# Kernel tuning notes

Hardware: AMD Instinct MI355X
Metric: run time of the kernel (lower is better)

Reference implementation:

```python
import jax, jax.numpy as jnp
import numpy as np

BN_EPS = 1e-5

def _conv(x, W, b, stride, pad):
    # x: [B,C,H,W], W: [O,I,kh,kw]
    y = jax.lax.conv_general_dilated(
        x, W, window_strides=(stride, stride),
        padding=[(pad, pad), (pad, pad)],
        dimension_numbers=('NCHW', 'OIHW', 'NCHW'))
    return y + b[None, :, None, None]

def _bn(x, gamma, beta, mean, var):
    inv = gamma * jax.lax.rsqrt(var + BN_EPS)
    return x * inv[None, :, None, None] + (beta - mean * inv)[None, :, None, None]

def _haar_cD(x):
    # pywt.dwt2(x, 'haar') diagonal detail over last two axes (even H,W):
    # cD[i,j] = (x[2i,2j] - x[2i,2j+1] - x[2i+1,2j] + x[2i+1,2j+1]) / 2
    a = x[..., 0::2, 0::2]
    b = x[..., 0::2, 1::2]
    c = x[..., 1::2, 0::2]
    d = x[..., 1::2, 1::2]
    return (a - b - c + d) * 0.5

def setup_inputs() -> dict:
    key = jax.random.key(0)
    ks = jax.random.split(key, 20)
    B = 8192
    f32 = jnp.float32
    inp = {
        'x':   jax.random.normal(ks[0], (B, 3, 32, 32), dtype=f32),
        # conv1: 3 -> 32, k5 s2 p2
        'w1':  jax.random.normal(ks[1], (32, 3, 5, 5), dtype=f32) * 0.05,
        'b1':  jnp.zeros((32,), f32),
        'g1':  jnp.ones((32,), f32),
        'be1': jnp.zeros((32,), f32),
        'm1':  jax.random.normal(ks[2], (32,), dtype=f32) * 0.1,
        'v1':  jax.random.uniform(ks[3], (32,), dtype=f32, minval=0.5, maxval=1.5),
        # conv2: 32 -> 64, k3 s2 p1
        'w2':  jax.random.normal(ks[4], (64, 32, 3, 3), dtype=f32) * 0.05,
        'b2':  jnp.zeros((64,), f32),
        'g2':  jnp.ones((64,), f32),
        'be2': jnp.zeros((64,), f32),
        'm2':  jax.random.normal(ks[5], (64,), dtype=f32) * 0.1,
        'v2':  jax.random.uniform(ks[6], (64,), dtype=f32, minval=0.5, maxval=1.5),
        # attention conv: 64 -> 1, k1
        'wa':  jax.random.normal(ks[7], (1, 64, 1, 1), dtype=f32) * 0.1,
        'ba':  jnp.zeros((1,), f32),
        # decoder linears (torch Linear layout: [out, in])
        'wd1': jax.random.normal(ks[8], (512, 64 * 8 * 8), dtype=f32) * 0.02,
        'bd1': jnp.zeros((512,), f32),
        'wd2': jax.random.normal(ks[9], (128, 512), dtype=f32) * 0.04,
        'bd2': jnp.zeros((128,), f32),
    }
    return inp

def reference(x, w1, b1, g1, be1, m1, v1, w2, b2, g2, be2, m2, v2,
              wa, ba, wd1, bd1, wd2, bd2):
    # wavelet_conv stem
    h = jax.nn.relu(_bn(_conv(x, w1, b1, 2, 2), g1, be1, m1, v1))   # [B,32,16,16]
    feat = jax.nn.relu(_bn(_conv(h, w2, b2, 2, 1), g2, be2, m2, v2))  # [B,64,8,8]
    # Haar DWT diagonal-detail gate (detached in the original)
    cD = jax.lax.stop_gradient(_haar_cD(feat))                        # [B,64,4,4]
    cD_up = jnp.repeat(jnp.repeat(cD, 2, axis=-2), 2, axis=-1)        # [B,64,8,8]
    feat = feat * cD_up
    # attention gate
    attn = jax.nn.sigmoid(_conv(feat, wa, ba, 1, 0))                  # [B,1,8,8]
    feat = feat * attn
    # decode
    f = feat.reshape(feat.shape[0], -1)                               # [B,4096]
    h1 = jax.nn.relu(f @ wd1.T + bd1)                                  # [B,512]
    return jax.nn.sigmoid(h1 @ wd2.T + bd2)                            # [B,128]
```

## Files before the change

### kernel.cpp

```cpp
#include <hip/hip_runtime.h>
#include <hip/hip_bf16.h>

typedef __bf16 bf16x8 __attribute__((ext_vector_type(8)));
typedef __bf16 bf16x4 __attribute__((ext_vector_type(4)));
typedef float f32x4 __attribute__((ext_vector_type(4)));

#define BN_EPS 1e-5f

__device__ __forceinline__ void gl_lds16(const __bf16* g, __bf16* l) {
    __builtin_amdgcn_global_load_lds(
        (const __attribute__((address_space(1))) unsigned int*)g,
        (__attribute__((address_space(3))) unsigned int*)l,
        16, 0, 0);
}

__global__ __launch_bounds__(256) void prep_all_kernel(
    const float* __restrict__ wd1, __bf16* __restrict__ wd1o,
    const float* __restrict__ wd2, const float* __restrict__ w1,
    const float* __restrict__ w2,
    __bf16* __restrict__ wd2o, __bf16* __restrict__ w1o,
    __bf16* __restrict__ w2o)
{
    __shared__ float t2[64][65];
    const int tid = threadIdx.x;
    if (blockIdx.x < 512) {
        const int n = blockIdx.x;
        const float* src = wd1 + (size_t)n * 4096;
        #pragma unroll
        for (int r = 0; r < 16; ++r) {
            int j = r * 256 + tid;
            t2[j & 63][j >> 6] = src[j];
        }
        __syncthreads();
        __bf16* dst = wd1o + (size_t)n * 4096;
        #pragma unroll
        for (int r = 0; r < 16; ++r) {
            int t = r * 256 + tid;
            dst[t] = (__bf16)t2[t >> 6][t & 63];
        }
        return;
    }
    int i = (blockIdx.x - 512) * 256 + tid;
    if (i < 65536) { wd2o[i] = (__bf16)wd2[i]; return; }
    i -= 65536;
    if (i < 4096) {
        int oc = i >> 7, rem = i & 127;
        int ot = rem >> 3, j = rem & 7;
        float v = 0.f;
        if (ot < 15 && j < 5) {
            int ic = ot / 5, ky = ot % 5;
            v = w1[((oc * 3 + ic) * 5 + ky) * 5 + j];
        }
        w1o[i] = (__bf16)v;
        return;
    }
    i -= 4096;
    if (i < 18432) {
        int oc = i / 288, rem = i % 288;
        int tap = rem / 32, ic = rem % 32;
        w2o[i] = (__bf16)w2[(oc * 32 + ic) * 9 + tap];
    }
}

__global__ __launch_bounds__(256, 5) void conv_fused_kernel(
    const float* __restrict__ x,
    const __bf16* __restrict__ w1r, const float* __restrict__ b1,
    const float* __restrict__ g1, const float* __restrict__ be1,
    const float* __restrict__ m1, const float* __restrict__ v1,
    const __bf16* __restrict__ w2r, const float* __restrict__ b2,
    const float* __restrict__ g2, const float* __restrict__ be2,
    const float* __restrict__ m2, const float* __restrict__ v2,
    const float* __restrict__ wa, const float* __restrict__ ba,
    __bf16* __restrict__ f)
{
    __shared__ __align__(16) __bf16 xsb[3 * 36 * 40];
    __shared__ __align__(16) char  ubuf[23552];
    __bf16* hsf  = (__bf16*)ubuf;
    float*  feat = (float*)ubuf;
    float*  cds  = (float*)(ubuf + 17408);
    float*  atn  = (float*)(ubuf + 22528);

    const int b    = blockIdx.x;
    const int tid  = threadIdx.x;
    const int lane = tid & 63;
    const int wave = tid >> 6;
    const int lo   = lane >> 4;
    const int ln   = lane & 15;

    {
        bf16x8 z = {};
        for (int i = tid; i < 540; i += 256) *(bf16x8*)&xsb[i * 8] = z;
        if (tid < 132) {
            int pi = tid >> 2, ch = tid & 3;
            int pix = (pi < 17) ? pi : (pi - 16) * 17;
            *(bf16x8*)&hsf[pix * 40 + ch * 8] = z;
        }
    }
    __syncthreads();

    {
        const float4* xb = (const float4*)(x + (size_t)b * 3072);
        #pragma unroll
        for (int r = 0; r < 3; ++r) {
            int c = r * 256 + tid;
            int plane = c >> 8, rem = c & 255;
            int row = rem >> 3, c4 = rem & 7;
            float4 v = xb[c];
            bf16x4 h;
            h[0] = (__bf16)v.x; h[1] = (__bf16)v.y; h[2] = (__bf16)v.z; h[3] = (__bf16)v.w;
            *(bf16x4*)&xsb[plane * 1440 + (row + 2) * 40 + 4 + c4 * 4] = h;
        }
    }

    bf16x8 bw1[2][4];
    #pragma unroll
    for (int nt = 0; nt < 2; ++nt)
        #pragma unroll
        for (int s = 0; s < 4; ++s)
            bw1[nt][s] = *(const bf16x8*)(w1r + (nt * 16 + ln) * 128 + (s * 4 + lo) * 8);
    __syncthreads();

    f32x4 c1[4][2] = {};
    const unsigned int* xw = (const unsigned int*)xsb;
    #pragma unroll
    for (int s = 0; s < 4; ++s) {
        const int o  = s * 4 + lo;
        const int ic = (o * 205) >> 10;
        const int ky = o - ic * 5;
        const bool dummy = (o == 15);
        const int icc = dummy ? 2 : ic;
        #pragma unroll
        for (int mt = 0; mt < 4; ++mt) {
            const int oy  = wave * 4 + mt;
            const int row = dummy ? 35 : (2 * oy + ky);
            const int dw  = icc * 720 + row * 20 + ln + 1;
            union { unsigned int u[4]; bf16x8 v; } fa;
            fa.u[0] = xw[dw]; fa.u[1] = xw[dw + 1]; fa.u[2] = xw[dw + 2]; fa.u[3] = 0;
            #pragma unroll
            for (int nt = 0; nt < 2; ++nt)
                c1[mt][nt] = __builtin_amdgcn_mfma_f32_16x16x32_bf16(fa.v, bw1[nt][s], c1[mt][nt], 0, 0, 0);
        }
    }

    #pragma unroll
    for (int nt = 0; nt < 2; ++nt) {
        const int oc  = nt * 16 + ln;
        const float inv = g1[oc] * rsqrtf(v1[oc] + BN_EPS);
        const float bb  = be1[oc] + (b1[oc] - m1[oc]) * inv;
        #pragma unroll
        for (int mt = 0; mt < 4; ++mt) {
            const int hy = wave * 4 + mt + 1;
            #pragma unroll
            for (int r = 0; r < 4; ++r) {
                const int hx = lo * 4 + r + 1;
                hsf[(hy * 17 + hx) * 40 + oc] = (__bf16)fmaxf(c1[mt][nt][r] * inv + bb, 0.f);
            }
        }
    }

    const int wm = wave >> 1, wn = wave & 1;
    bf16x8 bw2[2][9];
    #pragma unroll
    for (int nt = 0; nt < 2; ++nt) {
        const __bf16* wp = w2r + (wn * 32 + nt * 16 + ln) * 288 + lo * 8;
        #pragma unroll
        for (int ks = 0; ks < 9; ++ks)
            bw2[nt][ks] = *(const bf16x8*)(wp + ks * 32);
    }
    __syncthreads();

    f32x4 c2[2][2] = {};
    {
        int pixbase[2];
        #pragma unroll
        for (int mt = 0; mt < 2; ++mt) {
            int p = wm * 32 + mt * 16 + ln;
            int qy = p >> 3, qx = p & 7;
            pixbase[mt] = (2 * qy * 17 + 2 * qx) * 40 + lo * 8;
        }
        #pragma unroll
        for (int ks = 0; ks < 9; ++ks) {
            const int ty = ks / 3, tx = ks % 3;
            bf16x8 af[2];
            #pragma unroll
            for (int mt = 0; mt < 2; ++mt)
                af[mt] = *(const bf16x8*)&hsf[pixbase[mt] + (ty * 17 + tx) * 40];
            #pragma unroll
            for (int mt = 0; mt < 2; ++mt)
                #pragma unroll
                for (int nt = 0; nt < 2; ++nt)
                    c2[mt][nt] = __builtin_amdgcn_mfma_f32_16x16x32_bf16(af[mt], bw2[nt][ks], c2[mt][nt], 0, 0, 0);
        }
    }
    __syncthreads();

    #pragma unroll
    for (int nt = 0; nt < 2; ++nt) {
        const int oc  = wn * 32 + nt * 16 + ln;
        const float inv = g2[oc] * rsqrtf(v2[oc] + BN_EPS);
        const float bb  = be2[oc] + (b2[oc] - m2[oc]) * inv;
        #pragma unroll
        for (int mt = 0; mt < 2; ++mt) {
            const int p0 = wm * 32 + mt * 16 + lo * 4;
            f32x4 o;
            #pragma unroll
            for (int r = 0; r < 4; ++r)
                o[r] = fmaxf(c2[mt][nt][r] * inv + bb, 0.f);
            *(f32x4*)&feat[oc * 68 + p0] = o;
        }
    }
    __syncthreads();

    {
        const int c = tid >> 2, y = tid & 3;
        const float* fr = feat + c * 68 + 16 * y;
        f32x4 t0 = *(const f32x4*)(fr);
        f32x4 t2v = *(const f32x4*)(fr + 4);
        f32x4 t1 = *(const f32x4*)(fr + 8);
        f32x4 t3 = *(const f32x4*)(fr + 12);
        f32x4 o;
        o[0] = 0.5f * (t0[0] - t0[1] - t1[0] + t1[1]);
        o[1] = 0.5f * (t0[2] - t0[3] - t1[2] + t1[3]);
        o[2] = 0.5f * (t2v[0] - t2v[1] - t3[0] + t3[1]);
        o[3] = 0.5f * (t2v[2] - t2v[3] - t3[2] + t3[3]);
        *(f32x4*)&cds[c * 20 + y * 4] = o;
    }
    __syncthreads();

    const int q  = tid & 63;
    const int g  = wave;
    const int qy2 = q >> 3, qx2 = q & 7;
    const int qq = (qy2 >> 1) * 4 + (qx2 >> 1);
    float a2[16];
    float part = 0.f;
    #pragma unroll
    for (int j = 0; j < 16; ++j) {
        int oc = g * 16 + j;
        float v = feat[oc * 68 + q] * cds[oc * 20 + qq];
        a2[j] = v;
        part += v * wa[oc];
    }
    atn[g * 64 + q] = part;
    __syncthreads();
    float s2  = atn[q] + atn[64 + q] + atn[128 + q] + atn[192 + q] + ba[0];
    float sig = 1.f / (1.f + __expf(-s2));

    bf16x8 fo0, fo1;
    #pragma unroll
    for (int j = 0; j < 8; ++j) {
        fo0[j] = (__bf16)(a2[j] * sig);
        fo1[j] = (__bf16)(a2[j + 8] * sig);
    }
    __bf16* fb = f + (size_t)b * 4096 + q * 64 + g * 16;
    *(bf16x8*)fb = fo0;
    *(bf16x8*)(fb + 8) = fo1;
}

__global__ __launch_bounds__(256, 4) void gemm1_split_kernel(
    const __bf16* __restrict__ A, const __bf16* __restrict__ B,
    float* __restrict__ P)
{
    const int K = 4096, NOUT = 512, KH = 2048;
    __shared__ __align__(16) __bf16 As[64][64];
    __shared__ __align__(16) __bf16 Bs[128][64];
    const int tid  = threadIdx.x;
    const int lane = tid & 63;
    const int wave = tid >> 6;
    const int lo = lane >> 4, ln = lane & 15;
    const int bid = blockIdx.x;
    const int swz = (bid & 7) * 128 + (bid >> 3);
    const int n0  = (swz & 3) * 128;
    const int zz  = (swz >> 2) & 1;
    const int m0  = (swz >> 3) * 64;
    const int ks0 = zz * KH;
    const int sw = ln & 7;
    f32x4 acc[4][2] = {};
    for (int k0 = ks0; k0 < ks0 + KH; k0 += 64) {
        #pragma unroll
        for (int r = 0; r < 2; ++r) {
            int i = r * 256 + tid;
            int row = i >> 3, cs = i & 7;
            gl_lds16(A + (size_t)(m0 + row) * K + k0 + (cs ^ (row & 7)) * 8, &As[0][0] + i * 8);
        }
        #pragma unroll
        for (int r = 0; r < 4; ++r) {
            int i = r * 256 + tid;
            int row = i >> 3, cs = i & 7;
            gl_lds16(B + (size_t)(n0 + row) * K + k0 + (cs ^ (row & 7)) * 8, &Bs[0][0] + i * 8);
        }
        __syncthreads();
        #pragma unroll
        for (int s = 0; s < 2; ++s) {
            const int c = s * 4 + lo;
            const int slot = (c ^ sw) * 8;
            bf16x8 af[4], bfr[2];
            #pragma unroll
            for (int mt = 0; mt < 4; ++mt)
                af[mt] = *(const bf16x8*)(&As[mt * 16 + ln][slot]);
            #pragma unroll
            for (int nt = 0; nt < 2; ++nt)
                bfr[nt] = *(const bf16x8*)(&Bs[wave * 32 + nt * 16 + ln][slot]);
            #pragma unroll
            for (int mt = 0; mt < 4; ++mt)
                #pragma unroll
                for (int nt = 0; nt < 2; ++nt)
                    acc[mt][nt] = __builtin_amdgcn_mfma_f32_16x16x32_bf16(af[mt], bfr[nt], acc[mt][nt], 0, 0, 0);
        }
        __syncthreads();
    }
    float* Pp = P + (size_t)zz * 8192 * 512;
    #pragma unroll
    for (int mt = 0; mt < 4; ++mt)
        #pragma unroll
        for (int nt = 0; nt < 2; ++nt)
            #pragma unroll
            for (int r = 0; r < 4; ++r) {
                int m = m0 + mt * 16 + lo * 4 + r;
                int n = n0 + wave * 32 + nt * 16 + ln;
                Pp[(size_t)m * NOUT + n] = acc[mt][nt][r];
            }
}

__global__ __launch_bounds__(256) void gemm1_kernel(
    const __bf16* __restrict__ A, const __bf16* __restrict__ B,
    const float* __restrict__ bias, __bf16* __restrict__ C)
{
    const int K = 4096, NOUT = 512;
    __shared__ __align__(16) __bf16 As[64][64];
    __shared__ __align__(16) __bf16 Bs[128][64];
    const int tid  = threadIdx.x;
    const int lane = tid & 63;
    const int wave = tid >> 6;
    const int lo = lane >> 4, ln = lane & 15;
    const int bid = blockIdx.x;
    const int swz = (bid & 7) * 64 + (bid >> 3);
    const int n0  = (swz & 3) * 128;
    const int m0  = (swz >> 2) * 64;
    const int sw = ln & 7;
    f32x4 acc[4][2] = {};
    for (int k0 = 0; k0 < K; k0 += 64) {
        #pragma unroll
        for (int r = 0; r < 2; ++r) {
            int i = r * 256 + tid;
            int row = i >> 3, cs = i & 7;
            gl_lds16(A + (size_t)(m0 + row) * K + k0 + (cs ^ (row & 7)) * 8, &As[0][0] + i * 8);
        }
        #pragma unroll
        for (int r = 0; r < 4; ++r) {
            int i = r * 256 + tid;
            int row = i >> 3, cs = i & 7;
            gl_lds16(B + (size_t)(n0 + row) * K + k0 + (cs ^ (row & 7)) * 8, &Bs[0][0] + i * 8);
        }
        __syncthreads();
        #pragma unroll
        for (int s = 0; s < 2; ++s) {
            const int c = s * 4 + lo;
            const int slot = (c ^ sw) * 8;
            bf16x8 af[4], bfr[2];
            #pragma unroll
            for (int mt = 0; mt < 4; ++mt)
                af[mt] = *(const bf16x8*)(&As[mt * 16 + ln][slot]);
            #pragma unroll
            for (int nt = 0; nt < 2; ++nt)
                bfr[nt] = *(const bf16x8*)(&Bs[wave * 32 + nt * 16 + ln][slot]);
            #pragma unroll
            for (int mt = 0; mt < 4; ++mt)
                #pragma unroll
                for (int nt = 0; nt < 2; ++nt)
                    acc[mt][nt] = __builtin_amdgcn_mfma_f32_16x16x32_bf16(af[mt], bfr[nt], acc[mt][nt], 0, 0, 0);
        }
        __syncthreads();
    }
    #pragma unroll
    for (int mt = 0; mt < 4; ++mt)
        #pragma unroll
        for (int nt = 0; nt < 2; ++nt)
            #pragma unroll
            for (int r = 0; r < 4; ++r) {
                int m = m0 + mt * 16 + lo * 4 + r;
                int n = n0 + wave * 32 + nt * 16 + ln;
                float v = acc[mt][nt][r] + bias[n];
                C[(size_t)m * NOUT + n] = (__bf16)fmaxf(v, 0.f);
            }
}

__global__ __launch_bounds__(256, 4) void gemm2_kernel(
    const __bf16* __restrict__ A, const float* __restrict__ P,
    const float* __restrict__ bd1, const __bf16* __restrict__ B,
    const float* __restrict__ bias, float* __restrict__ Out, int fused)
{
    const int K = 512, NOUT = 128;
    __shared__ __align__(16) __bf16 As[32][64];
    __shared__ __align__(16) __bf16 Bs[128][64];
    const int tid  = threadIdx.x;
    const int lane = tid & 63;
    const int wave = tid >> 6;
    const int lo = lane >> 4, ln = lane & 15;
    const int m0 = blockIdx.x * 32;
    const int sw = ln & 7;
    const size_t HALF = (size_t)8192 * 512;
    f32x4 acc[2][2] = {};
    for (int k0 = 0; k0 < K; k0 += 64) {
        {
            int i = tid;
            int row = i >> 3, cs = i & 7;
            int k = k0 + (cs ^ (row & 7)) * 8;
            if (fused) {
                const float* p0 = P + (size_t)(m0 + row) * K + k;
                f32x4 a0 = *(const f32x4*)(p0);
                f32x4 a1 = *(const f32x4*)(p0 + 4);
                f32x4 c0 = *(const f32x4*)(p0 + HALF);
                f32x4 c1 = *(const f32x4*)(p0 + HALF + 4);
                f32x4 b0 = *(const f32x4*)(bd1 + k);
                f32x4 b1v = *(const f32x4*)(bd1 + k + 4);
                bf16x8 o;
                #pragma unroll
                for (int j = 0; j < 4; ++j) {
                    o[j]     = (__bf16)fmaxf(a0[j] + c0[j] + b0[j], 0.f);
                    o[j + 4] = (__bf16)fmaxf(a1[j] + c1[j] + b1v[j], 0.f);
                }
                *(bf16x8*)(&As[0][0] + i * 8) = o;
            } else {
                gl_lds16(A + (size_t)(m0 + row) * K + k, &As[0][0] + i * 8);
            }
        }
        #pragma unroll
        for (int r = 0; r < 4; ++r) {
            int i = r * 256 + tid;
            int row = i >> 3, cs = i & 7;
            gl_lds16(B + (size_t)row * K + k0 + (cs ^ (row & 7)) * 8, &Bs[0][0] + i * 8);
        }
        __syncthreads();
        #pragma unroll
        for (int s = 0; s < 2; ++s) {
            const int c = s * 4 + lo;
            const int slot = (c ^ sw) * 8;
            bf16x8 af[2], bfr[2];
            #pragma unroll
            for (int mt = 0; mt < 2; ++mt)
                af[mt] = *(const bf16x8*)(&As[mt * 16 + ln][slot]);
            #pragma unroll
            for (int nt = 0; nt < 2; ++nt)
                bfr[nt] = *(const bf16x8*)(&Bs[wave * 32 + nt * 16 + ln][slot]);
            #pragma unroll
            for (int mt = 0; mt < 2; ++mt)
                #pragma unroll
                for (int nt = 0; nt < 2; ++nt)
                    acc[mt][nt] = __builtin_amdgcn_mfma_f32_16x16x32_bf16(af[mt], bfr[nt], acc[mt][nt], 0, 0, 0);
        }
        __syncthreads();
    }
    #pragma unroll
    for (int mt = 0; mt < 2; ++mt)
        #pragma unroll
        for (int nt = 0; nt < 2; ++nt)
            #pragma unroll
            for (int r = 0; r < 4; ++r) {
                int m = m0 + mt * 16 + lo * 4 + r;
                int n = wave * 32 + nt * 16 + ln;
                float v = acc[mt][nt][r] + bias[n];
                Out[(size_t)m * NOUT + n] = 1.f / (1.f + __expf(-v));
            }
}

extern "C" void kernel_launch(void* const* d_in, const int* in_sizes, int n_in,
                              void* d_out, int out_size, void* d_ws, size_t ws_size,
                              hipStream_t stream)
{
    const float* x   = (const float*)d_in[0];
    const float* w1  = (const float*)d_in[1];
    const float* b1  = (const float*)d_in[2];
    const float* g1  = (const float*)d_in[3];
    const float* be1 = (const float*)d_in[4];
    const float* m1  = (const float*)d_in[5];
    const float* v1  = (const float*)d_in[6];
    const float* w2  = (const float*)d_in[7];
    const float* b2  = (const float*)d_in[8];
    const float* g2  = (const float*)d_in[9];
    const float* be2 = (const float*)d_in[10];
    const float* m2  = (const float*)d_in[11];
    const float* v2  = (const float*)d_in[12];
    const float* wa  = (const float*)d_in[13];
    const float* ba  = (const float*)d_in[14];
    const float* wd1 = (const float*)d_in[15];
    const float* bd1 = (const float*)d_in[16];
    const float* wd2 = (const float*)d_in[17];
    const float* bd2 = (const float*)d_in[18];

    char* ws = (char*)d_ws;
    const size_t SZ_F  = 67108864;
    const size_t SZ_P  = 33554432;
    const size_t SZ_H1 = 8388608;
    const bool use_split = ws_size >= (SZ_F + SZ_P + SZ_H1 + 4194304 + 131072 + 65536 + 8192);

    __bf16* f_bf = (__bf16*)ws;
    float*  P;
    __bf16* h1_bf;
    char* tail;
    if (use_split) {
        P      = (float*)(ws + SZ_F);
        h1_bf  = (__bf16*)(ws + SZ_F + SZ_P);
        tail   = ws + SZ_F + SZ_P + SZ_H1;
    } else {
        P      = nullptr;
        h1_bf  = (__bf16*)(ws + SZ_F);
        tail   = ws + SZ_F + SZ_H1;
    }
    __bf16* wd1_bf = (__bf16*)tail;
    __bf16* wd2_bf = (__bf16*)(tail + 4194304);
    __bf16* w2r_bf = (__bf16*)(tail + 4194304 + 131072);
    __bf16* w1r_bf = (__bf16*)(tail + 4194304 + 131072 + 65536);

    prep_all_kernel<<<856, 256, 0, stream>>>(wd1, wd1_bf, wd2, w1, w2, wd2_bf, w1r_bf, w2r_bf);

    conv_fused_kernel<<<8192, 256, 0, stream>>>(x, w1r_bf, b1, g1, be1, m1, v1,
                                                w2r_bf, b2, g2, be2, m2, v2, wa, ba, f_bf);

    if (use_split) {
        gemm1_split_kernel<<<1024, 256, 0, stream>>>(f_bf, wd1_bf, P);
        gemm2_kernel<<<256, 256, 0, stream>>>(nullptr, P, bd1, wd2_bf, bd2, (float*)d_out, 1);
    } else {
        gemm1_kernel<<<512, 256, 0, stream>>>(f_bf, wd1_bf, bd1, h1_bf);
        gemm2_kernel<<<256, 256, 0, stream>>>(h1_bf, nullptr, bd1, wd2_bf, bd2, (float*)d_out, 0);
    }
}
```

Baseline: 303.5 us.

## Replace global split-K partials with intra-block split-K reduced through LDS

The first decoder GEMM used to write two fp32 partial-sum buffers to global memory, which the second GEMM then read back, summed, and passed through bias and ReLU. It now runs 512-thread blocks in which two 256-thread groups each handle half of K. The groups reduce their partials through LDS, and the block writes bias+ReLU bf16 output directly. This removes the round trip of a 32MB fp32 intermediate and the fused-load path in gemm2, at the cost of larger blocks, 48KB of LDS per block, and an extra barrier.

```diff
diff --git a/kernel.cpp b/kernel.cpp
--- a/kernel.cpp
+++ b/kernel.cpp
@@ -256,37 +256,42 @@
     *(bf16x8*)(fb + 8) = fo1;
 }
 
-__global__ __launch_bounds__(256, 4) void gemm1_split_kernel(
+__global__ __launch_bounds__(512, 4) void gemm1_ib_kernel(
     const __bf16* __restrict__ A, const __bf16* __restrict__ B,
-    float* __restrict__ P)
+    const float* __restrict__ bias, __bf16* __restrict__ C)
 {
     const int K = 4096, NOUT = 512, KH = 2048;
-    __shared__ __align__(16) __bf16 As[64][64];
-    __shared__ __align__(16) __bf16 Bs[128][64];
+    __shared__ __align__(16) char lds[49152];
     const int tid  = threadIdx.x;
-    const int lane = tid & 63;
-    const int wave = tid >> 6;
-    const int lo = lane >> 4, ln = lane & 15;
+    const int grp  = tid >> 8;
+    const int lt   = tid & 255;
+    const int lane = lt & 63;
+    const int wv   = lt >> 6;
+    const int lo   = lane >> 4, ln = lane & 15;
+    __bf16* Asg = (__bf16*)lds + grp * 4096;
+    __bf16* Bsg = (__bf16*)(lds + 16384) + grp * 8192;
+
     const int bid = blockIdx.x;
-    const int swz = (bid & 7) * 128 + (bid >> 3);
+    const int swz = (bid & 7) * 64 + (bid >> 3);
     const int n0  = (swz & 3) * 128;
-    const int zz  = (swz >> 2) & 1;
-    const int m0  = (swz >> 3) * 64;
-    const int ks0 = zz * KH;
-    const int sw = ln & 7;
+    const int m0  = (swz >> 2) * 64;
+    const int kb  = grp * KH;
+    const int sw  = ln & 7;
+
     f32x4 acc[4][2] = {};
-    for (int k0 = ks0; k0 < ks0 + KH; k0 += 64) {
+    for (int k0 = 0; k0 < KH; k0 += 64) {
+        const int kk = kb + k0;
         #pragma unroll
         for (int r = 0; r < 2; ++r) {
-            int i = r * 256 + tid;
+            int i = r * 256 + lt;
             int row = i >> 3, cs = i & 7;
-            gl_lds16(A + (size_t)(m0 + row) * K + k0 + (cs ^ (row & 7)) * 8, &As[0][0] + i * 8);
+            gl_lds16(A + (size_t)(m0 + row) * K + kk + (cs ^ (row & 7)) * 8, Asg + i * 8);
         }
         #pragma unroll
         for (int r = 0; r < 4; ++r) {
-            int i = r * 256 + tid;
+            int i = r * 256 + lt;
             int row = i >> 3, cs = i & 7;
-            gl_lds16(B + (size_t)(n0 + row) * K + k0 + (cs ^ (row & 7)) * 8, &Bs[0][0] + i * 8);
+            gl_lds16(B + (size_t)(n0 + row) * K + kk + (cs ^ (row & 7)) * 8, Bsg + i * 8);
         }
         __syncthreads();
         #pragma unroll
@@ -296,10 +301,10 @@
             bf16x8 af[4], bfr[2];
             #pragma unroll
             for (int mt = 0; mt < 4; ++mt)
-                af[mt] = *(const bf16x8*)(&As[mt * 16 + ln][slot]);
+                af[mt] = *(const bf16x8*)(Asg + (mt * 16 + ln) * 64 + slot);
             #pragma unroll
             for (int nt = 0; nt < 2; ++nt)
-                bfr[nt] = *(const bf16x8*)(&Bs[wave * 32 + nt * 16 + ln][slot]);
+                bfr[nt] = *(const bf16x8*)(Bsg + (wv * 32 + nt * 16 + ln) * 64 + slot);
             #pragma unroll
             for (int mt = 0; mt < 4; ++mt)
                 #pragma unroll
@@ -308,86 +313,36 @@
         }
         __syncthreads();
     }
-    float* Pp = P + (size_t)zz * 8192 * 512;
-    #pragma unroll
-    for (int mt = 0; mt < 4; ++mt)
-        #pragma unroll
-        for (int nt = 0; nt < 2; ++nt)
-            #pragma unroll
-            for (int r = 0; r < 4; ++r) {
-                int m = m0 + mt * 16 + lo * 4 + r;
-                int n = n0 + wave * 32 + nt * 16 + ln;
-                Pp[(size_t)m * NOUT + n] = acc[mt][nt][r];
-            }
-}
-
-__global__ __launch_bounds__(256) void gemm1_kernel(
+
+    float* Ps = (float*)lds;
+    if (grp == 1) {
+        #pragma unroll
+        for (int mt = 0; mt < 4; ++mt)
+            #pragma unroll
+            for (int nt = 0; nt < 2; ++nt)
+                #pragma unroll
+                for (int r = 0; r < 4; ++r)
+                    Ps[(mt * 16 + lo * 4 + r) * 132 + wv * 32 + nt * 16 + ln] = acc[mt][nt][r];
+    }
+    __syncthreads();
+    if (grp == 0) {
+        #pragma unroll
+        for (int mt = 0; mt < 4; ++mt)
+            #pragma unroll
+            for (int nt = 0; nt < 2; ++nt)
+                #pragma unroll
+                for (int r = 0; r < 4; ++r) {
+                    const int ml = mt * 16 + lo * 4 + r;
+                    const int nl = wv * 32 + nt * 16 + ln;
+                    float v = acc[mt][nt][r] + Ps[ml * 132 + nl] + bias[n0 + nl];
+                    C[(size_t)(m0 + ml) * NOUT + n0 + nl] = (__bf16)fmaxf(v, 0.f);
+                }
+    }
+}
+
+__global__ __launch_bounds__(256, 4) void gemm2_kernel(
     const __bf16* __restrict__ A, const __bf16* __restrict__ B,
-    const float* __restrict__ bias, __bf16* __restrict__ C)
-{
-    const int K = 4096, NOUT = 512;
-    __shared__ __align__(16) __bf16 As[64][64];
-    __shared__ __align__(16) __bf16 Bs[128][64];
-    const int tid  = threadIdx.x;
-    const int lane = tid & 63;
-    const int wave = tid >> 6;
-    const int lo = lane >> 4, ln = lane & 15;
-    const int bid = blockIdx.x;
-    const int swz = (bid & 7) * 64 + (bid >> 3);
-    const int n0  = (swz & 3) * 128;
-    const int m0  = (swz >> 2) * 64;
-    const int sw = ln & 7;
-    f32x4 acc[4][2] = {};
-    for (int k0 = 0; k0 < K; k0 += 64) {
-        #pragma unroll
-        for (int r = 0; r < 2; ++r) {
-            int i = r * 256 + tid;
-            int row = i >> 3, cs = i & 7;
-            gl_lds16(A + (size_t)(m0 + row) * K + k0 + (cs ^ (row & 7)) * 8, &As[0][0] + i * 8);
-        }
-        #pragma unroll
-        for (int r = 0; r < 4; ++r) {
-            int i = r * 256 + tid;
-            int row = i >> 3, cs = i & 7;
-            gl_lds16(B + (size_t)(n0 + row) * K + k0 + (cs ^ (row & 7)) * 8, &Bs[0][0] + i * 8);
-        }
-        __syncthreads();
-        #pragma unroll
-        for (int s = 0; s < 2; ++s) {
-            const int c = s * 4 + lo;
-            const int slot = (c ^ sw) * 8;
-            bf16x8 af[4], bfr[2];
-            #pragma unroll
-            for (int mt = 0; mt < 4; ++mt)
-                af[mt] = *(const bf16x8*)(&As[mt * 16 + ln][slot]);
-            #pragma unroll
-            for (int nt = 0; nt < 2; ++nt)
-                bfr[nt] = *(const bf16x8*)(&Bs[wave * 32 + nt * 16 + ln][slot]);
-            #pragma unroll
-            for (int mt = 0; mt < 4; ++mt)
-                #pragma unroll
-                for (int nt = 0; nt < 2; ++nt)
-                    acc[mt][nt] = __builtin_amdgcn_mfma_f32_16x16x32_bf16(af[mt], bfr[nt], acc[mt][nt], 0, 0, 0);
-        }
-        __syncthreads();
-    }
-    #pragma unroll
-    for (int mt = 0; mt < 4; ++mt)
-        #pragma unroll
-        for (int nt = 0; nt < 2; ++nt)
-            #pragma unroll
-            for (int r = 0; r < 4; ++r) {
-                int m = m0 + mt * 16 + lo * 4 + r;
-                int n = n0 + wave * 32 + nt * 16 + ln;
-                float v = acc[mt][nt][r] + bias[n];
-                C[(size_t)m * NOUT + n] = (__bf16)fmaxf(v, 0.f);
-            }
-}
-
-__global__ __launch_bounds__(256, 4) void gemm2_kernel(
-    const __bf16* __restrict__ A, const float* __restrict__ P,
-    const float* __restrict__ bd1, const __bf16* __restrict__ B,
-    const float* __restrict__ bias, float* __restrict__ Out, int fused)
+    const float* __restrict__ bias, float* __restrict__ Out)
 {
     const int K = 512, NOUT = 128;
     __shared__ __align__(16) __bf16 As[32][64];
@@ -398,31 +353,12 @@
     const int lo = lane >> 4, ln = lane & 15;
     const int m0 = blockIdx.x * 32;
     const int sw = ln & 7;
-    const size_t HALF = (size_t)8192 * 512;
     f32x4 acc[2][2] = {};
     for (int k0 = 0; k0 < K; k0 += 64) {
         {
             int i = tid;
             int row = i >> 3, cs = i & 7;
-            int k = k0 + (cs ^ (row & 7)) * 8;
-            if (fused) {
-                const float* p0 = P + (size_t)(m0 + row) * K + k;
-                f32x4 a0 = *(const f32x4*)(p0);
-                f32x4 a1 = *(const f32x4*)(p0 + 4);
-                f32x4 c0 = *(const f32x4*)(p0 + HALF);
-                f32x4 c1 = *(const f32x4*)(p0 + HALF + 4);
-                f32x4 b0 = *(const f32x4*)(bd1 + k);
-                f32x4 b1v = *(const f32x4*)(bd1 + k + 4);
-                bf16x8 o;
-                #pragma unroll
-                for (int j = 0; j < 4; ++j) {
-                    o[j]     = (__bf16)fmaxf(a0[j] + c0[j] + b0[j], 0.f);
-                    o[j + 4] = (__bf16)fmaxf(a1[j] + c1[j] + b1v[j], 0.f);
-                }
-                *(bf16x8*)(&As[0][0] + i * 8) = o;
-            } else {
-                gl_lds16(A + (size_t)(m0 + row) * K + k, &As[0][0] + i * 8);
-            }
+            gl_lds16(A + (size_t)(m0 + row) * K + k0 + (cs ^ (row & 7)) * 8, &As[0][0] + i * 8);
         }
         #pragma unroll
         for (int r = 0; r < 4; ++r) {
@@ -489,23 +425,11 @@
 
     char* ws = (char*)d_ws;
     const size_t SZ_F  = 67108864;
-    const size_t SZ_P  = 33554432;
     const size_t SZ_H1 = 8388608;
-    const bool use_split = ws_size >= (SZ_F + SZ_P + SZ_H1 + 4194304 + 131072 + 65536 + 8192);
-
-    __bf16* f_bf = (__bf16*)ws;
-    float*  P;
-    __bf16* h1_bf;
-    char* tail;
-    if (use_split) {
-        P      = (float*)(ws + SZ_F);
-        h1_bf  = (__bf16*)(ws + SZ_F + SZ_P);
-        tail   = ws + SZ_F + SZ_P + SZ_H1;
-    } else {
-        P      = nullptr;
-        h1_bf  = (__bf16*)(ws + SZ_F);
-        tail   = ws + SZ_F + SZ_H1;
-    }
+
+    __bf16* f_bf  = (__bf16*)ws;
+    __bf16* h1_bf = (__bf16*)(ws + SZ_F);
+    char*   tail  = ws + SZ_F + SZ_H1;
     __bf16* wd1_bf = (__bf16*)tail;
     __bf16* wd2_bf = (__bf16*)(tail + 4194304);
     __bf16* w2r_bf = (__bf16*)(tail + 4194304 + 131072);
@@ -516,11 +440,7 @@
     conv_fused_kernel<<<8192, 256, 0, stream>>>(x, w1r_bf, b1, g1, be1, m1, v1,
                                                 w2r_bf, b2, g2, be2, m2, v2, wa, ba, f_bf);
 
-    if (use_split) {
-        gemm1_split_kernel<<<1024, 256, 0, stream>>>(f_bf, wd1_bf, P);
-        gemm2_kernel<<<256, 256, 0, stream>>>(nullptr, P, bd1, wd2_bf, bd2, (float*)d_out, 1);
-    } else {
-        gemm1_kernel<<<512, 256, 0, stream>>>(f_bf, wd1_bf, bd1, h1_bf);
-        gemm2_kernel<<<256, 256, 0, stream>>>(h1_bf, nullptr, bd1, wd2_bf, bd2, (float*)d_out, 0);
-    }
-}
+    gemm1_ib_kernel<<<512, 512, 0, stream>>>(f_bf, wd1_bf, bd1, h1_bf);
+
+    gemm2_kernel<<<256, 256, 0, stream>>>(h1_bf, wd2_bf, bd2, (float*)d_out);
+}
```

Result: faster. 296.5 us, median of 2 (-2.3%).

## Double-buffer LDS tiles in split-K GEMM1 to overlap loads with MFMA

Applied to the files above, without the earlier changes.

Converts the split-K first decoder GEMM from a single-buffered load-sync-compute loop to a two-stage LDS ping-pong pipeline. The next K-tile is issued with global_load_lds while the current tile is consumed, using partial vmcnt waits and raw s_barrier instead of full __syncthreads. This targets global-load latency stalls, at the cost of doubling LDS per block and lowering the occupancy hint from 4 to 3 blocks per CU.

```diff
diff --git a/kernel.cpp b/kernel.cpp
--- a/kernel.cpp
+++ b/kernel.cpp
@@ -256,13 +256,13 @@
     *(bf16x8*)(fb + 8) = fo1;
 }
 
-__global__ __launch_bounds__(256, 4) void gemm1_split_kernel(
+__global__ __launch_bounds__(256, 3) void gemm1_split_kernel(
     const __bf16* __restrict__ A, const __bf16* __restrict__ B,
     float* __restrict__ P)
 {
     const int K = 4096, NOUT = 512, KH = 2048;
-    __shared__ __align__(16) __bf16 As[64][64];
-    __shared__ __align__(16) __bf16 Bs[128][64];
+    __shared__ __align__(16) __bf16 As[2][64][64];
+    __shared__ __align__(16) __bf16 Bs[2][128][64];
     const int tid  = threadIdx.x;
     const int lane = tid & 63;
     const int wave = tid >> 6;
@@ -273,22 +273,25 @@
     const int zz  = (swz >> 2) & 1;
     const int m0  = (swz >> 3) * 64;
     const int ks0 = zz * KH;
-    const int sw = ln & 7;
+    const int sw  = ln & 7;
+
     f32x4 acc[4][2] = {};
-    for (int k0 = ks0; k0 < ks0 + KH; k0 += 64) {
+
+    auto STAGE = [&](int k0, int bb) {
         #pragma unroll
         for (int r = 0; r < 2; ++r) {
             int i = r * 256 + tid;
             int row = i >> 3, cs = i & 7;
-            gl_lds16(A + (size_t)(m0 + row) * K + k0 + (cs ^ (row & 7)) * 8, &As[0][0] + i * 8);
+            gl_lds16(A + (size_t)(m0 + row) * K + k0 + (cs ^ (row & 7)) * 8, &As[bb][0][0] + i * 8);
         }
         #pragma unroll
         for (int r = 0; r < 4; ++r) {
             int i = r * 256 + tid;
             int row = i >> 3, cs = i & 7;
-            gl_lds16(B + (size_t)(n0 + row) * K + k0 + (cs ^ (row & 7)) * 8, &Bs[0][0] + i * 8);
-        }
-        __syncthreads();
+            gl_lds16(B + (size_t)(n0 + row) * K + k0 + (cs ^ (row & 7)) * 8, &Bs[bb][0][0] + i * 8);
+        }
+    };
+    auto COMPUTE = [&](int bb) {
         #pragma unroll
         for (int s = 0; s < 2; ++s) {
             const int c = s * 4 + lo;
@@ -296,18 +299,34 @@
             bf16x8 af[4], bfr[2];
             #pragma unroll
             for (int mt = 0; mt < 4; ++mt)
-                af[mt] = *(const bf16x8*)(&As[mt * 16 + ln][slot]);
+                af[mt] = *(const bf16x8*)(&As[bb][mt * 16 + ln][slot]);
             #pragma unroll
             for (int nt = 0; nt < 2; ++nt)
-                bfr[nt] = *(const bf16x8*)(&Bs[wave * 32 + nt * 16 + ln][slot]);
+                bfr[nt] = *(const bf16x8*)(&Bs[bb][wave * 32 + nt * 16 + ln][slot]);
             #pragma unroll
             for (int mt = 0; mt < 4; ++mt)
                 #pragma unroll
                 for (int nt = 0; nt < 2; ++nt)
                     acc[mt][nt] = __builtin_amdgcn_mfma_f32_16x16x32_bf16(af[mt], bfr[nt], acc[mt][nt], 0, 0, 0);
         }
-        __syncthreads();
-    }
+    };
+
+    STAGE(ks0, 0);
+    for (int t = 0; t < 31; ++t) {
+        STAGE(ks0 + (t + 1) * 64, (t + 1) & 1);
+        asm volatile("s_waitcnt vmcnt(6)" ::: "memory");
+        __builtin_amdgcn_sched_barrier(0);
+        __builtin_amdgcn_s_barrier();
+        COMPUTE(t & 1);
+        asm volatile("s_waitcnt lgkmcnt(0)" ::: "memory");
+        __builtin_amdgcn_sched_barrier(0);
+        __builtin_amdgcn_s_barrier();
+    }
+    asm volatile("s_waitcnt vmcnt(0)" ::: "memory");
+    __builtin_amdgcn_sched_barrier(0);
+    __builtin_amdgcn_s_barrier();
+    COMPUTE(1);
+
     float* Pp = P + (size_t)zz * 8192 * 512;
     #pragma unroll
     for (int mt = 0; mt < 4; ++mt)
```

Result: slower. 317.9 us (+4.8%).
